# Performance work log

Measured on AMD Instinct MI355X. Metric: run time of the kernel, lower is better.

The kernel has to match this reference:

```python
import jax, jax.numpy as jnp
import numpy as np

D_MODEL = 256
D_HEAD = 64
N_HEAD = 8


def setup_inputs() -> dict:
    key = jax.random.key(0)
    ks = jax.random.split(key, 8)
    b, h, w = 32, 64, 64
    dk = D_HEAD * N_HEAD
    s = 1.0 / np.sqrt(D_MODEL)
    x = jax.random.normal(ks[0], (b, D_MODEL, h, w), dtype=jnp.float32)
    query = jax.random.normal(ks[1], (b, D_MODEL), dtype=jnp.float32)
    Wkv = jax.random.uniform(ks[2], (2 * dk, D_MODEL), jnp.float32, -s, s)
    bkv = jax.random.uniform(ks[3], (2 * dk,), jnp.float32, -s, s)
    Wq = jax.random.uniform(ks[4], (dk, D_MODEL), jnp.float32, -s, s)
    bq = jax.random.uniform(ks[5], (dk,), jnp.float32, -s, s)
    sf = 1.0 / np.sqrt(dk)
    Wfc = jax.random.uniform(ks[6], (D_MODEL, dk), jnp.float32, -sf, sf)
    bfc = jax.random.uniform(ks[7], (D_MODEL,), jnp.float32, -sf, sf)
    return {"x": x, "query": query, "Wkv": Wkv, "bkv": bkv, "Wq": Wq, "bq": bq, "Wfc": Wfc, "bfc": bfc}


def reference(x, query, Wkv, bkv, Wq, bq, Wfc, bfc):
    b, c, h, w = x.shape
    t = h * w
    scale = 1.0 / np.sqrt(D_HEAD).astype(np.float32)
    # 1x1 conv == per-pixel linear: (b, 2*n*d, t)
    kv = jnp.einsum('bchw,oc->bohw', x, Wkv).reshape(b, 2 * N_HEAD, D_HEAD, t)
    kv = kv + bkv.reshape(1, 2 * N_HEAD, D_HEAD, 1)
    k, v = kv[:, :N_HEAD], kv[:, N_HEAD:]  # each (b, n, d, t)
    q = (query @ Wq.T + bq).reshape(b, N_HEAD, D_HEAD)
    logits = jnp.einsum('bnd,bndj->bnj', q, k) * scale
    attn = jax.nn.softmax(logits, axis=2)
    out = jnp.einsum('bnj,bndj->bnd', attn, v).reshape(b, N_HEAD * D_HEAD)
    return jax.nn.relu(out @ Wfc.T + bfc)
```

## Files before the change

### kernel.cpp

```cpp
#include <hip/hip_runtime.h>
#include <hip/hip_bf16.h>


#define B_     32
#define C_     256
#define T_     4096
#define NH_    8
#define DH_    64

__global__ __launch_bounds__(256) void k_prep(
    const float* __restrict__ query, const float* __restrict__ Wkv,
    const float* __restrict__ bkv, const float* __restrict__ Wq,
    const float* __restrict__ bq, float* __restrict__ qWt,
    float* __restrict__ qb) {
  const int hb = blockIdx.x;
  const int b  = blockIdx.y;
  const int t  = threadIdx.x;
  __shared__ float qrow_s[C_];
  __shared__ float qsh[256];

  qrow_s[t] = query[(size_t)b * C_ + t];
  __syncthreads();

  {
    const int o = hb * 256 + t;
    const float* wrow = Wq + (size_t)o * C_;
    float s = bq[o];
    #pragma unroll 8
    for (int c = 0; c < C_; c += 4) {
      float4 w = *(const float4*)(wrow + c);
      s += w.x * qrow_s[c] + w.y * qrow_s[c + 1] + w.z * qrow_s[c + 2] + w.w * qrow_s[c + 3];
    }
    qsh[t] = s;
  }
  __syncthreads();

  const float scale = 0.125f;
  {
    const int c = t;
    float acc[4] = {0.f, 0.f, 0.f, 0.f};
    #pragma unroll 2
    for (int dd = 0; dd < DH_; ++dd) {
      #pragma unroll
      for (int nl = 0; nl < 4; ++nl) {
        const int row = (hb * 4 + nl) * DH_ + dd;
        acc[nl] += qsh[nl * DH_ + dd] * Wkv[(size_t)row * C_ + c];
      }
    }
    #pragma unroll
    for (int nl = 0; nl < 4; ++nl)
      qWt[((size_t)b * C_ + c) * NH_ + hb * 4 + nl] = acc[nl] * scale;
  }
  if (t < 4) {
    const int n = hb * 4 + t;
    float s = 0.f;
    #pragma unroll 8
    for (int dd = 0; dd < DH_; ++dd)
      s += qsh[t * DH_ + dd] * bkv[n * DH_ + dd];
    qb[b * NH_ + n] = s * scale;
  }
}

__global__ __launch_bounds__(256) void k_logits(
    const float* __restrict__ x, const float* __restrict__ qWt,
    const float* __restrict__ qbv, float* __restrict__ logits) {
  const int b = blockIdx.y;
  const int t = threadIdx.x;
  const int j = blockIdx.x * 512 + t * 2;
  __shared__ float qws[C_ * NH_];

  #pragma unroll
  for (int r = 0; r < 8; ++r) qws[r * 256 + t] = qWt[(size_t)b * (C_ * NH_) + r * 256 + t];
  __syncthreads();

  const float* xb = x + (size_t)b * C_ * T_ + j;
  const float* qb = qbv + b * NH_;

  float acc0[NH_], acc1[NH_];
  #pragma unroll
  for (int n = 0; n < NH_; ++n) { acc0[n] = qb[n]; acc1[n] = qb[n]; }

  #pragma unroll 4
  for (int c = 0; c < C_; ++c) {
    const float2 xv = *(const float2*)(xb + (size_t)c * T_);
    const float4 w0 = *(const float4*)(qws + c * 8);
    const float4 w1 = *(const float4*)(qws + c * 8 + 4);
    acc0[0] += w0.x * xv.x; acc1[0] += w0.x * xv.y;
    acc0[1] += w0.y * xv.x; acc1[1] += w0.y * xv.y;
    acc0[2] += w0.z * xv.x; acc1[2] += w0.z * xv.y;
    acc0[3] += w0.w * xv.x; acc1[3] += w0.w * xv.y;
    acc0[4] += w1.x * xv.x; acc1[4] += w1.x * xv.y;
    acc0[5] += w1.y * xv.x; acc1[5] += w1.y * xv.y;
    acc0[6] += w1.z * xv.x; acc1[6] += w1.z * xv.y;
    acc0[7] += w1.w * xv.x; acc1[7] += w1.w * xv.y;
  }

  float* lg = logits + (size_t)b * NH_ * T_ + j;
  #pragma unroll
  for (int n = 0; n < NH_; ++n) {
    float2 o; o.x = acc0[n]; o.y = acc1[n];
    *(float2*)(lg + (size_t)n * T_) = o;
  }
}

__global__ __launch_bounds__(256) void k_softmax(float* __restrict__ lg) {
  float* p = lg + (size_t)blockIdx.x * T_;
  const int t = threadIdx.x;
  float4 v[4];
  #pragma unroll
  for (int i = 0; i < 4; ++i) v[i] = *(const float4*)(p + t * 4 + i * 1024);

  float m = -3.4e38f;
  #pragma unroll
  for (int i = 0; i < 4; ++i)
    m = fmaxf(m, fmaxf(fmaxf(v[i].x, v[i].y), fmaxf(v[i].z, v[i].w)));
  #pragma unroll
  for (int o = 32; o >= 1; o >>= 1) m = fmaxf(m, __shfl_xor(m, o));
  __shared__ float sm[4];
  if ((t & 63) == 0) sm[t >> 6] = m;
  __syncthreads();
  m = fmaxf(fmaxf(sm[0], sm[1]), fmaxf(sm[2], sm[3]));

  float s = 0.f;
  #pragma unroll
  for (int i = 0; i < 4; ++i) {
    v[i].x = expf(v[i].x - m); v[i].y = expf(v[i].y - m);
    v[i].z = expf(v[i].z - m); v[i].w = expf(v[i].w - m);
    s += v[i].x + v[i].y + v[i].z + v[i].w;
  }
  #pragma unroll
  for (int o = 32; o >= 1; o >>= 1) s += __shfl_xor(s, o);
  __shared__ float ss[4];
  if ((t & 63) == 0) ss[t >> 6] = s;
  __syncthreads();
  s = ss[0] + ss[1] + ss[2] + ss[3];
  const float inv = 1.0f / s;

  #pragma unroll
  for (int i = 0; i < 4; ++i) {
    v[i].x *= inv; v[i].y *= inv; v[i].z *= inv; v[i].w *= inv;
    *(float4*)(p + t * 4 + i * 1024) = v[i];
  }
}

#define BJ_  256
#define BJS_ 32
#define XPITCH_ 33
__global__ __launch_bounds__(256) void k_xattn(
    const float* __restrict__ x, const float* __restrict__ attn,
    float* __restrict__ part) {
  const int jt = blockIdx.x;
  const int b  = blockIdx.y;
  const int j0 = jt * BJ_;
  const int t  = threadIdx.x;
  __shared__ float xs[C_ * XPITCH_];
  __shared__ float at[BJ_ * NH_];

  const float* xb = x + (size_t)b * C_ * T_;
  const float* ab = attn + (size_t)b * NH_ * T_;

  #pragma unroll
  for (int n = 0; n < NH_; ++n) at[t * NH_ + n] = ab[(size_t)n * T_ + j0 + t];

  float acc[NH_];
  #pragma unroll
  for (int n = 0; n < NH_; ++n) acc[n] = 0.f;

  const int cr = t >> 3;
  const int jc = (t & 7) * 4;

  for (int sIt = 0; sIt < BJ_ / BJS_; ++sIt) {
    const int js = j0 + sIt * BJS_;
    __syncthreads();
    #pragma unroll
    for (int p = 0; p < 8; ++p) {
      const int c = cr + p * 32;
      float4 vv = *(const float4*)(xb + (size_t)c * T_ + js + jc);
      float* dst = &xs[c * XPITCH_ + jc];
      dst[0] = vv.x; dst[1] = vv.y; dst[2] = vv.z; dst[3] = vv.w;
    }
    __syncthreads();
    const float* xr = &xs[t * XPITCH_];
    const float* ar = &at[sIt * BJS_ * NH_];
    #pragma unroll 4
    for (int jj = 0; jj < BJS_; ++jj) {
      const float xv = xr[jj];
      const float4 w0 = *(const float4*)(ar + jj * 8);
      const float4 w1 = *(const float4*)(ar + jj * 8 + 4);
      acc[0] += w0.x * xv; acc[1] += w0.y * xv;
      acc[2] += w0.z * xv; acc[3] += w0.w * xv;
      acc[4] += w1.x * xv; acc[5] += w1.y * xv;
      acc[6] += w1.z * xv; acc[7] += w1.w * xv;
    }
  }

  float* pb = part + ((size_t)b * 16 + jt) * (NH_ * C_);
  #pragma unroll
  for (int n = 0; n < NH_; ++n) pb[n * C_ + t] = acc[n];
}

__global__ __launch_bounds__(512) void k_finish(
    const float* __restrict__ part, const float* __restrict__ Wkv,
    const float* __restrict__ bkv, const float* __restrict__ Wfc,
    const float* __restrict__ bfc, float* __restrict__ out) {
  __shared__ float xattn[NH_ * C_];
  __shared__ float outv[512];
  const int b = blockIdx.x;
  const int t = threadIdx.x;

  const float* pb = part + (size_t)b * 16 * (NH_ * C_);
  for (int idx = t; idx < NH_ * C_; idx += 512) {
    float s = 0.f;
    #pragma unroll
    for (int jt = 0; jt < 16; ++jt) s += pb[(size_t)jt * (NH_ * C_) + idx];
    xattn[idx] = s;
  }
  __syncthreads();

  {
    const int o = t;
    const int n = o >> 6;
    const float* wrow = Wkv + (size_t)(512 + o) * C_;
    const float* xa = &xattn[n * C_];
    float s = bkv[512 + o];
    #pragma unroll 8
    for (int c = 0; c < C_; c += 4) {
      float4 w = *(const float4*)(wrow + c);
      s += w.x * xa[c] + w.y * xa[c + 1] + w.z * xa[c + 2] + w.w * xa[c + 3];
    }
    outv[o] = s;
  }
  __syncthreads();

  if (t < 256) {
    const int m = t;
    const float* wrow = Wfc + (size_t)m * 512;
    float s = bfc[m];
    #pragma unroll 8
    for (int o = 0; o < 512; o += 4) {
      float4 w = *(const float4*)(wrow + o);
      s += w.x * outv[o] + w.y * outv[o + 1] + w.z * outv[o + 2] + w.w * outv[o + 3];
    }
    out[(size_t)b * 256 + m] = fmaxf(s, 0.f);
  }
}

extern "C" void kernel_launch(void* const* d_in, const int* in_sizes, int n_in,
                              void* d_out, int out_size, void* d_ws, size_t ws_size,
                              hipStream_t stream) {
  const float* x     = (const float*)d_in[0];
  const float* query = (const float*)d_in[1];
  const float* Wkv   = (const float*)d_in[2];
  const float* bkv   = (const float*)d_in[3];
  const float* Wq    = (const float*)d_in[4];
  const float* bq    = (const float*)d_in[5];
  const float* Wfc   = (const float*)d_in[6];
  const float* bfc   = (const float*)d_in[7];
  float* out = (float*)d_out;
  float* ws  = (float*)d_ws;

  float* qWt    = ws;
  float* qb     = ws + 65536;
  float* logits = ws + 65792;
  float* part   = ws + 1114368;

  k_prep   <<<dim3(2,  B_), 256, 0, stream>>>(query, Wkv, bkv, Wq, bq, qWt, qb);
  k_logits <<<dim3(8,  B_), 256, 0, stream>>>(x, qWt, qb, logits);
  k_softmax<<<B_ * NH_,     256, 0, stream>>>(logits);
  k_xattn  <<<dim3(16, B_), 256, 0, stream>>>(x, logits, part);
  k_finish <<<B_,           512, 0, stream>>>(part, Wkv, bkv, Wfc, bfc, out);
}
```

Measured before the change: 297.2 us.

## Split reductions across more blocks in prep, logits, and finish kernels

k_prep now runs one block per head instead of one per four heads. k_logits splits the channel reduction into two halves, giving twice as many blocks and batched x loads; the softmax kernel sums the two partial logit buffers. The finish stage is split into a k_outv kernel over two block groups plus a separate k_fc kernel, and k_xattn reads attention weights straight from global memory instead of staging them in LDS. The goal is more parallelism and better latency hiding on a GPU with many CUs. The cost is extra partial-logit traffic and one more kernel launch.

```diff
diff --git a/kernel.cpp b/kernel.cpp
--- a/kernel.cpp
+++ b/kernel.cpp
@@ -1,6 +1,5 @@
 #include <hip/hip_runtime.h>
 #include <hip/hip_bf16.h>
-
 
 #define B_     32
 #define C_     256
@@ -13,89 +12,98 @@
     const float* __restrict__ bkv, const float* __restrict__ Wq,
     const float* __restrict__ bq, float* __restrict__ qWt,
     float* __restrict__ qb) {
-  const int hb = blockIdx.x;
-  const int b  = blockIdx.y;
-  const int t  = threadIdx.x;
+  const int n = blockIdx.x;
+  const int b = blockIdx.y;
+  const int t = threadIdx.x;
   __shared__ float qrow_s[C_];
-  __shared__ float qsh[256];
+  __shared__ float psum[4 * 64];
+  __shared__ float qsh[64];
+  __shared__ float pb_s[64];
 
   qrow_s[t] = query[(size_t)b * C_ + t];
   __syncthreads();
 
   {
-    const int o = hb * 256 + t;
-    const float* wrow = Wq + (size_t)o * C_;
-    float s = bq[o];
-    #pragma unroll 8
-    for (int c = 0; c < C_; c += 4) {
+    const int d = t & 63, ch = t >> 6;
+    const float* wrow = Wq + (size_t)(n * DH_ + d) * C_ + ch * 64;
+    const float* qr = qrow_s + ch * 64;
+    float s = 0.f;
+    #pragma unroll
+    for (int c = 0; c < 64; c += 4) {
       float4 w = *(const float4*)(wrow + c);
-      s += w.x * qrow_s[c] + w.y * qrow_s[c + 1] + w.z * qrow_s[c + 2] + w.w * qrow_s[c + 3];
-    }
-    qsh[t] = s;
-  }
+      s += w.x * qr[c] + w.y * qr[c + 1] + w.z * qr[c + 2] + w.w * qr[c + 3];
+    }
+    psum[ch * 64 + d] = s;
+  }
+  __syncthreads();
+  if (t < 64)
+    qsh[t] = bq[n * DH_ + t] + psum[t] + psum[64 + t] + psum[128 + t] + psum[192 + t];
   __syncthreads();
 
   const float scale = 0.125f;
   {
-    const int c = t;
-    float acc[4] = {0.f, 0.f, 0.f, 0.f};
-    #pragma unroll 2
-    for (int dd = 0; dd < DH_; ++dd) {
-      #pragma unroll
-      for (int nl = 0; nl < 4; ++nl) {
-        const int row = (hb * 4 + nl) * DH_ + dd;
-        acc[nl] += qsh[nl * DH_ + dd] * Wkv[(size_t)row * C_ + c];
-      }
-    }
-    #pragma unroll
-    for (int nl = 0; nl < 4; ++nl)
-      qWt[((size_t)b * C_ + c) * NH_ + hb * 4 + nl] = acc[nl] * scale;
-  }
-  if (t < 4) {
-    const int n = hb * 4 + t;
+    const float* wk = Wkv + (size_t)(n * DH_) * C_ + t;
+    float acc = 0.f;
+    #pragma unroll 8
+    for (int dd = 0; dd < DH_; ++dd) acc += qsh[dd] * wk[(size_t)dd * C_];
+    qWt[((size_t)b * C_ + t) * NH_ + n] = acc * scale;
+  }
+  if (t < 64) pb_s[t] = qsh[t] * bkv[n * DH_ + t];
+  __syncthreads();
+  if (t == 0) {
     float s = 0.f;
     #pragma unroll 8
-    for (int dd = 0; dd < DH_; ++dd)
-      s += qsh[t * DH_ + dd] * bkv[n * DH_ + dd];
+    for (int dd = 0; dd < 64; ++dd) s += pb_s[dd];
     qb[b * NH_ + n] = s * scale;
   }
 }
 
 __global__ __launch_bounds__(256) void k_logits(
     const float* __restrict__ x, const float* __restrict__ qWt,
-    const float* __restrict__ qbv, float* __restrict__ logits) {
-  const int b = blockIdx.y;
+    const float* __restrict__ qbv, float* __restrict__ lgpart) {
+  const int half = blockIdx.y;
+  const int b = blockIdx.z;
   const int t = threadIdx.x;
   const int j = blockIdx.x * 512 + t * 2;
-  __shared__ float qws[C_ * NH_];
-
-  #pragma unroll
-  for (int r = 0; r < 8; ++r) qws[r * 256 + t] = qWt[(size_t)b * (C_ * NH_) + r * 256 + t];
-  __syncthreads();
-
-  const float* xb = x + (size_t)b * C_ * T_ + j;
+  __shared__ float qws[128 * NH_];
+
+  {
+    const float4 v = *(const float4*)(qWt + (size_t)b * (C_ * NH_) + half * 1024 + t * 4);
+    *(float4*)(qws + t * 4) = v;
+  }
+  __syncthreads();
+
+  const float* xb = x + (size_t)b * C_ * T_ + (size_t)(half * 128) * T_ + j;
   const float* qb = qbv + b * NH_;
 
   float acc0[NH_], acc1[NH_];
   #pragma unroll
-  for (int n = 0; n < NH_; ++n) { acc0[n] = qb[n]; acc1[n] = qb[n]; }
-
-  #pragma unroll 4
-  for (int c = 0; c < C_; ++c) {
-    const float2 xv = *(const float2*)(xb + (size_t)c * T_);
-    const float4 w0 = *(const float4*)(qws + c * 8);
-    const float4 w1 = *(const float4*)(qws + c * 8 + 4);
-    acc0[0] += w0.x * xv.x; acc1[0] += w0.x * xv.y;
-    acc0[1] += w0.y * xv.x; acc1[1] += w0.y * xv.y;
-    acc0[2] += w0.z * xv.x; acc1[2] += w0.z * xv.y;
-    acc0[3] += w0.w * xv.x; acc1[3] += w0.w * xv.y;
-    acc0[4] += w1.x * xv.x; acc1[4] += w1.x * xv.y;
-    acc0[5] += w1.y * xv.x; acc1[5] += w1.y * xv.y;
-    acc0[6] += w1.z * xv.x; acc1[6] += w1.z * xv.y;
-    acc0[7] += w1.w * xv.x; acc1[7] += w1.w * xv.y;
-  }
-
-  float* lg = logits + (size_t)b * NH_ * T_ + j;
+  for (int n = 0; n < NH_; ++n) {
+    const float init = half ? 0.f : qb[n];
+    acc0[n] = init; acc1[n] = init;
+  }
+
+  for (int c0 = 0; c0 < 128; c0 += 8) {
+    float2 xv[8];
+    #pragma unroll
+    for (int cc = 0; cc < 8; ++cc)
+      xv[cc] = *(const float2*)(xb + (size_t)(c0 + cc) * T_);
+    #pragma unroll
+    for (int cc = 0; cc < 8; ++cc) {
+      const float4 w0 = *(const float4*)(qws + (c0 + cc) * 8);
+      const float4 w1 = *(const float4*)(qws + (c0 + cc) * 8 + 4);
+      acc0[0] += w0.x * xv[cc].x; acc1[0] += w0.x * xv[cc].y;
+      acc0[1] += w0.y * xv[cc].x; acc1[1] += w0.y * xv[cc].y;
+      acc0[2] += w0.z * xv[cc].x; acc1[2] += w0.z * xv[cc].y;
+      acc0[3] += w0.w * xv[cc].x; acc1[3] += w0.w * xv[cc].y;
+      acc0[4] += w1.x * xv[cc].x; acc1[4] += w1.x * xv[cc].y;
+      acc0[5] += w1.y * xv[cc].x; acc1[5] += w1.y * xv[cc].y;
+      acc0[6] += w1.z * xv[cc].x; acc1[6] += w1.z * xv[cc].y;
+      acc0[7] += w1.w * xv[cc].x; acc1[7] += w1.w * xv[cc].y;
+    }
+  }
+
+  float* lg = lgpart + (((size_t)half * B_ + b) * NH_) * T_ + j;
   #pragma unroll
   for (int n = 0; n < NH_; ++n) {
     float2 o; o.x = acc0[n]; o.y = acc1[n];
@@ -103,12 +111,20 @@
   }
 }
 
-__global__ __launch_bounds__(256) void k_softmax(float* __restrict__ lg) {
-  float* p = lg + (size_t)blockIdx.x * T_;
+__global__ __launch_bounds__(256) void k_softmax(
+    const float* __restrict__ lgpart, float* __restrict__ attn) {
+  const size_t row = blockIdx.x;
+  const float* p0 = lgpart + row * T_;
+  const float* p1 = lgpart + ((size_t)B_ * NH_ + row) * T_;
+  float* pa = attn + row * T_;
   const int t = threadIdx.x;
   float4 v[4];
   #pragma unroll
-  for (int i = 0; i < 4; ++i) v[i] = *(const float4*)(p + t * 4 + i * 1024);
+  for (int i = 0; i < 4; ++i) {
+    float4 a = *(const float4*)(p0 + t * 4 + i * 1024);
+    float4 c = *(const float4*)(p1 + t * 4 + i * 1024);
+    v[i].x = a.x + c.x; v[i].y = a.y + c.y; v[i].z = a.z + c.z; v[i].w = a.w + c.w;
+  }
 
   float m = -3.4e38f;
   #pragma unroll
@@ -139,7 +155,7 @@
   #pragma unroll
   for (int i = 0; i < 4; ++i) {
     v[i].x *= inv; v[i].y *= inv; v[i].z *= inv; v[i].w *= inv;
-    *(float4*)(p + t * 4 + i * 1024) = v[i];
+    *(float4*)(pa + t * 4 + i * 1024) = v[i];
   }
 }
 
@@ -154,13 +170,9 @@
   const int j0 = jt * BJ_;
   const int t  = threadIdx.x;
   __shared__ float xs[C_ * XPITCH_];
-  __shared__ float at[BJ_ * NH_];
 
   const float* xb = x + (size_t)b * C_ * T_;
-  const float* ab = attn + (size_t)b * NH_ * T_;
-
-  #pragma unroll
-  for (int n = 0; n < NH_; ++n) at[t * NH_ + n] = ab[(size_t)n * T_ + j0 + t];
+  const float* ab = attn + (size_t)b * NH_ * T_ + j0;
 
   float acc[NH_];
   #pragma unroll
@@ -170,27 +182,24 @@
   const int jc = (t & 7) * 4;
 
   for (int sIt = 0; sIt < BJ_ / BJS_; ++sIt) {
-    const int js = j0 + sIt * BJS_;
+    const int js = sIt * BJS_;
     __syncthreads();
     #pragma unroll
     for (int p = 0; p < 8; ++p) {
       const int c = cr + p * 32;
-      float4 vv = *(const float4*)(xb + (size_t)c * T_ + js + jc);
+      float4 vv = *(const float4*)(xb + (size_t)c * T_ + j0 + js + jc);
       float* dst = &xs[c * XPITCH_ + jc];
       dst[0] = vv.x; dst[1] = vv.y; dst[2] = vv.z; dst[3] = vv.w;
     }
     __syncthreads();
     const float* xr = &xs[t * XPITCH_];
-    const float* ar = &at[sIt * BJS_ * NH_];
     #pragma unroll 4
     for (int jj = 0; jj < BJS_; ++jj) {
       const float xv = xr[jj];
-      const float4 w0 = *(const float4*)(ar + jj * 8);
-      const float4 w1 = *(const float4*)(ar + jj * 8 + 4);
-      acc[0] += w0.x * xv; acc[1] += w0.y * xv;
-      acc[2] += w0.z * xv; acc[3] += w0.w * xv;
-      acc[4] += w1.x * xv; acc[5] += w1.y * xv;
-      acc[6] += w1.z * xv; acc[7] += w1.w * xv;
+      const int j = js + jj;
+      #pragma unroll
+      for (int n = 0; n < NH_; ++n)
+        acc[n] += ab[(size_t)n * T_ + j] * xv;
     }
   }
 
@@ -199,50 +208,55 @@
   for (int n = 0; n < NH_; ++n) pb[n * C_ + t] = acc[n];
 }
 
-__global__ __launch_bounds__(512) void k_finish(
+__global__ __launch_bounds__(256) void k_outv(
     const float* __restrict__ part, const float* __restrict__ Wkv,
-    const float* __restrict__ bkv, const float* __restrict__ Wfc,
+    const float* __restrict__ bkv, float* __restrict__ outvG) {
+  __shared__ float xa_s[4 * C_];
+  const int hb = blockIdx.x;
+  const int b  = blockIdx.y;
+  const int t  = threadIdx.x;
+
+  const float* pb = part + (size_t)b * 16 * (NH_ * C_) + hb * (4 * C_);
+  #pragma unroll
+  for (int r = 0; r < 4; ++r) {
+    const int idx = r * 256 + t;
+    float s = 0.f;
+    #pragma unroll
+    for (int jt = 0; jt < 16; ++jt) s += pb[(size_t)jt * (NH_ * C_) + idx];
+    xa_s[idx] = s;
+  }
+  __syncthreads();
+
+  const int o = hb * 256 + t;
+  const float* wrow = Wkv + (size_t)(512 + o) * C_;
+  const float* xa = &xa_s[(t >> 6) * C_];
+  float s = bkv[512 + o];
+  #pragma unroll 8
+  for (int c = 0; c < C_; c += 4) {
+    float4 w = *(const float4*)(wrow + c);
+    s += w.x * xa[c] + w.y * xa[c + 1] + w.z * xa[c + 2] + w.w * xa[c + 3];
+  }
+  outvG[(size_t)b * 512 + o] = s;
+}
+
+__global__ __launch_bounds__(256) void k_fc(
+    const float* __restrict__ outvG, const float* __restrict__ Wfc,
     const float* __restrict__ bfc, float* __restrict__ out) {
-  __shared__ float xattn[NH_ * C_];
-  __shared__ float outv[512];
+  __shared__ float ov[512];
   const int b = blockIdx.x;
   const int t = threadIdx.x;
-
-  const float* pb = part + (size_t)b * 16 * (NH_ * C_);
-  for (int idx = t; idx < NH_ * C_; idx += 512) {
-    float s = 0.f;
-    #pragma unroll
-    for (int jt = 0; jt < 16; ++jt) s += pb[(size_t)jt * (NH_ * C_) + idx];
-    xattn[idx] = s;
-  }
-  __syncthreads();
-
-  {
-    const int o = t;
-    const int n = o >> 6;
-    const float* wrow = Wkv + (size_t)(512 + o) * C_;
-    const float* xa = &xattn[n * C_];
-    float s = bkv[512 + o];
-    #pragma unroll 8
-    for (int c = 0; c < C_; c += 4) {
-      float4 w = *(const float4*)(wrow + c);
-      s += w.x * xa[c] + w.y * xa[c + 1] + w.z * xa[c + 2] + w.w * xa[c + 3];
-    }
-    outv[o] = s;
-  }
-  __syncthreads();
-
-  if (t < 256) {
-    const int m = t;
-    const float* wrow = Wfc + (size_t)m * 512;
-    float s = bfc[m];
-    #pragma unroll 8
-    for (int o = 0; o < 512; o += 4) {
-      float4 w = *(const float4*)(wrow + o);
-      s += w.x * outv[o] + w.y * outv[o + 1] + w.z * outv[o + 2] + w.w * outv[o + 3];
-    }
-    out[(size_t)b * 256 + m] = fmaxf(s, 0.f);
-  }
+  ov[t] = outvG[(size_t)b * 512 + t];
+  ov[256 + t] = outvG[(size_t)b * 512 + 256 + t];
+  __syncthreads();
+
+  const float* wrow = Wfc + (size_t)t * 512;
+  float s = bfc[t];
+  #pragma unroll 8
+  for (int o = 0; o < 512; o += 4) {
+    float4 w = *(const float4*)(wrow + o);
+    s += w.x * ov[o] + w.y * ov[o + 1] + w.z * ov[o + 2] + w.w * ov[o + 3];
+  }
+  out[(size_t)b * 256 + t] = fmaxf(s, 0.f);
 }
 
 extern "C" void kernel_launch(void* const* d_in, const int* in_sizes, int n_in,
@@ -261,12 +275,15 @@
 
   float* qWt    = ws;
   float* qb     = ws + 65536;
-  float* logits = ws + 65792;
-  float* part   = ws + 1114368;
-
-  k_prep   <<<dim3(2,  B_), 256, 0, stream>>>(query, Wkv, bkv, Wq, bq, qWt, qb);
-  k_logits <<<dim3(8,  B_), 256, 0, stream>>>(x, qWt, qb, logits);
-  k_softmax<<<B_ * NH_,     256, 0, stream>>>(logits);
-  k_xattn  <<<dim3(16, B_), 256, 0, stream>>>(x, logits, part);
-  k_finish <<<B_,           512, 0, stream>>>(part, Wkv, bkv, Wfc, bfc, out);
-}
+  float* lgpart = ws + 66048;
+  float* attn   = ws + 2163200;
+  float* part   = ws + 3211776;
+  float* outvG  = ws + 4260352;
+
+  k_prep   <<<dim3(NH_, B_),   256, 0, stream>>>(query, Wkv, bkv, Wq, bq, qWt, qb);
+  k_logits <<<dim3(8, 2, B_),  256, 0, stream>>>(x, qWt, qb, lgpart);
+  k_softmax<<<B_ * NH_,        256, 0, stream>>>(lgpart, attn);
+  k_xattn  <<<dim3(16, B_),    256, 0, stream>>>(x, attn, part);
+  k_outv   <<<dim3(2, B_),     256, 0, stream>>>(part, Wkv, bkv, outvG);
+  k_fc     <<<B_,              256, 0, stream>>>(outvG, Wfc, bfc, out);
+}
```

Result: faster. 274.3 us (-7.7%).
